# Kernel tuning notes

Measured on AMD Instinct MI355X. Metric: run time of the kernel, lower is better.

The kernel has to match this reference:

```python
import jax, jax.numpy as jnp
import numpy as np

V, I, H = 32000, 512, 1024
B, L, T = 8, 128, 256


def setup_inputs() -> dict:
    key = jax.random.key(0)
    ks = jax.random.split(key, 12)
    s = lambda k, shape, sc: jax.random.normal(k, shape, jnp.float32) * sc
    return {
        "input": jax.random.randint(ks[0], (B, L), 0, V),
        "targets": jax.random.randint(ks[1], (B, T), 0, V),
        "embed_w": s(ks[2], (V, I), 1.0),
        "Wih0": s(ks[3], (3 * H, I), 0.03),
        "Whh0": s(ks[4], (3 * H, H), 0.03),
        "bih0": jnp.zeros((3 * H,), jnp.float32),
        "bhh0": jnp.zeros((3 * H,), jnp.float32),
        "Wih1": s(ks[5], (3 * H, H), 0.03),
        "Whh1": s(ks[6], (3 * H, H), 0.03),
        "bih1": jnp.zeros((3 * H,), jnp.float32),
        "bhh1": jnp.zeros((3 * H,), jnp.float32),
        "Wc": s(ks[7], (H, 2 * H), 0.02),
        "bc": jnp.zeros((H,), jnp.float32),
        "Wv": s(ks[8], (V, H), 0.02),
        "bv": jnp.zeros((V,), jnp.float32),
    }


def _gru_layer(x, Wih, Whh, bih, bhh):
    # x: (B, S, in) -> (B, S, H). PyTorch gate order: r, z, n.
    Bn = x.shape[0]
    Hh = Whh.shape[1]

    def step(h, xt):
        gi = xt @ Wih.T + bih
        gh = h @ Whh.T + bhh
        ir, iz, ig = jnp.split(gi, 3, axis=-1)
        hr, hz, hg = jnp.split(gh, 3, axis=-1)
        r = jax.nn.sigmoid(ir + hr)
        z = jax.nn.sigmoid(iz + hz)
        n = jnp.tanh(ig + r * hg)
        hnew = (1.0 - z) * n + z * h
        return hnew, hnew

    h0 = jnp.zeros((Bn, Hh), x.dtype)
    _, ys = jax.lax.scan(step, h0, jnp.swapaxes(x, 0, 1))
    return jnp.swapaxes(ys, 0, 1)


def reference(input, targets, embed_w, Wih0, Whh0, bih0, bhh0, Wih1, Whh1, bih1, bhh1, Wc, bc, Wv, bv):
    # forcing = 1.0 (fully teacher-forced): GRU inputs = [prompt, targets[:, :-1]]
    Lp = input.shape[1]
    Tt = targets.shape[1]
    toks = jnp.concatenate([input, targets[:, :-1]], axis=1)  # (B, L+T-1)
    emb = embed_w[toks]                                       # (B, L+T-1, I)
    h1 = _gru_layer(emb, Wih0, Whh0, bih0, bhh0)
    O = _gru_layer(h1, Wih1, Whh1, bih1, bhh1)                # (B, L+T-1, H)

    # attention at decode step q: predicted = O[:, L-1+q], previous = O[:, :L-1+q]
    Q = O[:, Lp - 1:, :]                                      # (B, T, H)
    S = jnp.einsum('bqh,bkh->bqk', Q, O)                      # (B, T, L+T-1)
    k_idx = jnp.arange(O.shape[1])
    q_idx = jnp.arange(Tt)
    mask = k_idx[None, :] < (Lp - 1 + q_idx)[:, None]         # strict causal
    S = jnp.where(mask[None], S, -jnp.inf)
    A = jax.nn.softmax(S, axis=-1)
    ctx = jnp.einsum('bqk,bkh->bqh', A, O)                    # (B, T, H)
    comb = jnp.tanh(jnp.concatenate([Q, ctx], axis=-1) @ Wc.T + bc)
    logits = comb @ Wv.T + bv                                 # (B, T, V)
    return logits
```

## Files before the change

### kernel.cpp

```cpp
#include <hip/hip_runtime.h>

typedef __attribute__((ext_vector_type(8))) short bf16x8;
typedef __attribute__((ext_vector_type(4))) float f32x4;

#define GLOAD_LDS16(g, l)                                                     \
  __builtin_amdgcn_global_load_lds(                                           \
      (const __attribute__((address_space(1))) void*)(g),                     \
      (__attribute__((address_space(3))) void*)(l), 16, 0, 0)

#define ALOAD64(p)  __hip_atomic_load((p), __ATOMIC_RELAXED, __HIP_MEMORY_SCOPE_AGENT)
#define ALOADU32(p) __hip_atomic_load((p), __ATOMIC_RELAXED, __HIP_MEMORY_SCOPE_AGENT)
#define ASTOREU32(p, v) __hip_atomic_store((p), (v), __ATOMIC_RELAXED, __HIP_MEMORY_SCOPE_AGENT)

__device__ __forceinline__ unsigned short f2b(float f) {
  union { float f; unsigned int i; } v; v.f = f;
  unsigned int u = v.i;
  u += 0x7fffu + ((u >> 16) & 1u);
  return (unsigned short)(u >> 16);
}
__device__ __forceinline__ float sigm(float x) { return 1.f / (1.f + expf(-x)); }

#define HH   1024
#define H3   3072
#define BB   8
#define SP   384
#define SL   383
#define VV   32000
#define II   512
#define MQ   2048

#define TAG(s) ((unsigned)((s) + 1))

#define CB0 393216
#define CB1 1179648
#define CB2 1966080
#define CB3 2752512
#define CB4 3276800
#define CB5 11468800
__global__ void k_cvt_all(const float* __restrict__ s0, const float* __restrict__ s1,
                          const float* __restrict__ s2, const float* __restrict__ s3,
                          const float* __restrict__ s4, const float* __restrict__ s5,
                          unsigned short* __restrict__ dst) {
  for (int i = blockIdx.x * 256 + threadIdx.x; i < CB5; i += 2048 * 256) {
    const float* src; int o;
    if (i < CB0)      { src = s0; o = i; }
    else if (i < CB1) { src = s1; o = i - CB0; }
    else if (i < CB2) { src = s2; o = i - CB1; }
    else if (i < CB3) { src = s3; o = i - CB2; }
    else if (i < CB4) { src = s4; o = i - CB3; }
    else              { src = s5; o = i - CB4; }
    float4 v = ((const float4*)src)[o];
    ushort4 q;
    q.x = f2b(v.x); q.y = f2b(v.y); q.z = f2b(v.z); q.w = f2b(v.w);
    ((ushort4*)dst)[i] = q;
  }
}

__global__ void k_zero_u32(unsigned int* p, int n) {
  int i = blockIdx.x * 256 + threadIdx.x;
  if (i < n) p[i] = 0u;
}

__global__ void k_embed(const int* __restrict__ input, const int* __restrict__ targets,
                        const float* __restrict__ embed_w, unsigned short* __restrict__ emb) {
  int m = blockIdx.x;
  int b = m / SP, s = m % SP;
  unsigned short* dst = emb + (size_t)m * II;
  if (s == SL) {
    for (int i = threadIdx.x; i < II; i += 256) dst[i] = 0;
    return;
  }
  int tok = (s < 128) ? input[b * 128 + s] : targets[b * 256 + (s - 128)];
  const float* srcw = embed_w + (size_t)tok * II;
  for (int i = threadIdx.x; i < II; i += 256) dst[i] = f2b(srcw[i]);
}

template<bool TANH, bool OUTBF16>
__global__ __launch_bounds__(256) void k_gemm_bt(
    const unsigned short* __restrict__ A, const unsigned short* __restrict__ W,
    const float* __restrict__ bias, void* __restrict__ Cout,
    int M, int N, int K) {
  __shared__ __align__(16) unsigned short As[2][128 * 32];
  __shared__ __align__(16) unsigned short Ws[2][128 * 32];
  const int tid = threadIdx.x;
  const int gx = gridDim.x;
  const int nwg = gx * gridDim.y;
  int orig = blockIdx.y * gx + blockIdx.x;
  int wg = ((nwg & 7) == 0) ? ((orig & 7) * (nwg >> 3) + (orig >> 3)) : orig;
  const int mBase = (wg / gx) * 128, nBase = (wg % gx) * 128;
  const int wid = tid >> 6, lane = tid & 63;
  const int wr = wid >> 1, wc = wid & 1;
  f32x4 acc[4][4];
#pragma unroll
  for (int i = 0; i < 4; ++i)
#pragma unroll
    for (int j = 0; j < 4; ++j) acc[i][j] = (f32x4){0.f, 0.f, 0.f, 0.f};

  const int r0 = tid >> 2, c0 = (tid & 3) * 8;
  const int kq8 = (lane >> 4) * 8;

  auto stage = [&](int kt, int b) {
#pragma unroll
    for (int pass = 0; pass < 2; ++pass) {
      int r = pass * 64 + r0;
      GLOAD_LDS16(A + (size_t)(mBase + r) * K + kt + c0, &As[b][r * 32 + c0]);
      GLOAD_LDS16(W + (size_t)(nBase + r) * K + kt + c0, &Ws[b][r * 32 + c0]);
    }
  };

  stage(0, 0);
  int cur = 0;
  for (int kt = 0; kt < K; kt += 32) {
    asm volatile("s_waitcnt vmcnt(0)" ::: "memory");
    __syncthreads();
    if (kt + 32 < K) stage(kt + 32, cur ^ 1);
    bf16x8 af[4], bfr[4];
#pragma unroll
    for (int mf = 0; mf < 4; ++mf)
      af[mf] = *(const bf16x8*)&As[cur][(wr * 64 + mf * 16 + (lane & 15)) * 32 + kq8];
#pragma unroll
    for (int nf = 0; nf < 4; ++nf)
      bfr[nf] = *(const bf16x8*)&Ws[cur][(wc * 64 + nf * 16 + (lane & 15)) * 32 + kq8];
#pragma unroll
    for (int mf = 0; mf < 4; ++mf)
#pragma unroll
      for (int nf = 0; nf < 4; ++nf)
        acc[mf][nf] = __builtin_amdgcn_mfma_f32_16x16x32_bf16(af[mf], bfr[nf], acc[mf][nf], 0, 0, 0);
    cur ^= 1;
  }
  const int rq = (lane >> 4) * 4;
#pragma unroll
  for (int mf = 0; mf < 4; ++mf) {
#pragma unroll
    for (int nf = 0; nf < 4; ++nf) {
      int n = nBase + wc * 64 + nf * 16 + (lane & 15);
      float bvv = bias[n];
#pragma unroll
      for (int i = 0; i < 4; ++i) {
        int m = mBase + wr * 64 + mf * 16 + rq + i;
        float v = acc[mf][nf][i] + bvv;
        if (TANH) v = tanhf(v);
        if (OUTBF16) ((unsigned short*)Cout)[(size_t)m * N + n] = f2b(v);
        else         ((float*)Cout)[(size_t)m * N + n] = v;
      }
    }
  }
}

__global__ __launch_bounds__(256) void k_obf(const float* __restrict__ O,
                                             unsigned short* __restrict__ Obf,
                                             unsigned short* __restrict__ ObfT) {
  __shared__ unsigned short t[32][33];
  const int b = blockIdx.z, k0 = blockIdx.y * 32, h0 = blockIdx.x * 32;
  const int tx = threadIdx.x & 31, ty = threadIdx.x >> 5;
  const float* Ob = O + ((size_t)b * SP + k0) * 1024 + h0;
#pragma unroll
  for (int i = 0; i < 32; i += 8) {
    unsigned short q = f2b(Ob[(size_t)(ty + i) * 1024 + tx]);
    Obf[((size_t)b * SP + k0 + ty + i) * 1024 + h0 + tx] = q;
    t[ty + i][tx] = q;
  }
  __syncthreads();
#pragma unroll
  for (int i = 0; i < 32; i += 8)
    ObfT[((size_t)b * 1024 + h0 + ty + i) * SP + k0 + tx] = t[tx][ty + i];
}

__global__ void k_qcopy(const unsigned short* __restrict__ Obf,
                        unsigned short* __restrict__ X) {
  int row = blockIdx.x;
  int b = row >> 8, q = row & 255;
  const unsigned* src = (const unsigned*)(Obf + ((size_t)b * SP + 127 + q) * 1024);
  unsigned* dst = (unsigned*)(X + (size_t)row * 2048);
  for (int i = threadIdx.x; i < 512; i += 256) dst[i] = src[i];
}

__global__ __launch_bounds__(256) void k_gemm_qk(
    const unsigned short* __restrict__ Obf, float* __restrict__ Sout) {
  const int b = blockIdx.z;
  const unsigned short* A = Obf + (size_t)b * 393216 + 127 * 1024;
  const unsigned short* W = Obf + (size_t)b * 393216;
  float* Cout = Sout + (size_t)b * 98304;
  const int K = 1024, N = 384;
  __shared__ __align__(16) unsigned short As[2][128 * 32];
  __shared__ __align__(16) unsigned short Ws[2][128 * 32];
  const int tid = threadIdx.x;
  const int mBase = blockIdx.y * 128, nBase = blockIdx.x * 128;
  const int wid = tid >> 6, lane = tid & 63;
  const int wr = wid >> 1, wc = wid & 1;
  f32x4 acc[4][4];
#pragma unroll
  for (int i = 0; i < 4; ++i)
#pragma unroll
    for (int j = 0; j < 4; ++j) acc[i][j] = (f32x4){0.f, 0.f, 0.f, 0.f};
  const int r0 = tid >> 2, c0 = (tid & 3) * 8;
  const int kq8 = (lane >> 4) * 8;
  auto stage = [&](int kt, int bb) {
#pragma unroll
    for (int pass = 0; pass < 2; ++pass) {
      int r = pass * 64 + r0;
      GLOAD_LDS16(A + (size_t)(mBase + r) * K + kt + c0, &As[bb][r * 32 + c0]);
      GLOAD_LDS16(W + (size_t)(nBase + r) * K + kt + c0, &Ws[bb][r * 32 + c0]);
    }
  };
  stage(0, 0);
  int cur = 0;
  for (int kt = 0; kt < K; kt += 32) {
    asm volatile("s_waitcnt vmcnt(0)" ::: "memory");
    __syncthreads();
    if (kt + 32 < K) stage(kt + 32, cur ^ 1);
    bf16x8 af[4], bfr[4];
#pragma unroll
    for (int mf = 0; mf < 4; ++mf)
      af[mf] = *(const bf16x8*)&As[cur][(wr * 64 + mf * 16 + (lane & 15)) * 32 + kq8];
#pragma unroll
    for (int nf = 0; nf < 4; ++nf)
      bfr[nf] = *(const bf16x8*)&Ws[cur][(wc * 64 + nf * 16 + (lane & 15)) * 32 + kq8];
#pragma unroll
    for (int mf = 0; mf < 4; ++mf)
#pragma unroll
      for (int nf = 0; nf < 4; ++nf)
        acc[mf][nf] = __builtin_amdgcn_mfma_f32_16x16x32_bf16(af[mf], bfr[nf], acc[mf][nf], 0, 0, 0);
    cur ^= 1;
  }
  const int rq = (lane >> 4) * 4;
#pragma unroll
  for (int mf = 0; mf < 4; ++mf)
#pragma unroll
    for (int nf = 0; nf < 4; ++nf) {
      int n = nBase + wc * 64 + nf * 16 + (lane & 15);
#pragma unroll
      for (int i = 0; i < 4; ++i) {
        int m = mBase + wr * 64 + mf * 16 + rq + i;
        Cout[(size_t)m * N + n] = acc[mf][nf][i];
      }
    }
}

__global__ __launch_bounds__(64) void k_sm(const float* __restrict__ S,
                                           unsigned short* __restrict__ P) {
  const int row = blockIdx.x;
  const int q = row & 255;
  const int lim = 127 + q;
  const float* Sr = S + (size_t)row * SP;
  unsigned short* Pr = P + (size_t)row * SP;
  const int lane = threadIdx.x;
  float v[6];
  float mx = -INFINITY;
#pragma unroll
  for (int i = 0; i < 6; ++i) {
    int k = lane + i * 64;
    float x = (k < lim) ? Sr[k] : -INFINITY;
    v[i] = x; mx = fmaxf(mx, x);
  }
#pragma unroll
  for (int m = 1; m < 64; m <<= 1) mx = fmaxf(mx, __shfl_xor(mx, m));
  float sum = 0.f;
#pragma unroll
  for (int i = 0; i < 6; ++i) {
    float e = (v[i] == -INFINITY) ? 0.f : expf(v[i] - mx);
    v[i] = e; sum += e;
  }
#pragma unroll
  for (int m = 1; m < 64; m <<= 1) sum += __shfl_xor(sum, m);
  float rinv = 1.f / sum;
#pragma unroll
  for (int i = 0; i < 6; ++i) Pr[lane + i * 64] = f2b(v[i] * rinv);
}

__global__ __launch_bounds__(256) void k_gemm_pv(
    const unsigned short* __restrict__ Pbf, const unsigned short* __restrict__ ObfT,
    unsigned short* __restrict__ X) {
  const int b = blockIdx.z;
  const unsigned short* A = Pbf + (size_t)b * 98304;
  const unsigned short* W = ObfT + (size_t)b * 393216;
  unsigned short* Cout = X + (size_t)(b * 256) * 2048 + 1024;
  const int K = SP, N = 1024;
  __shared__ __align__(16) unsigned short As[2][128 * 32];
  __shared__ __align__(16) unsigned short Ws[2][128 * 32];
  const int tid = threadIdx.x;
  const int mBase = blockIdx.y * 128, nBase = blockIdx.x * 128;
  const int wid = tid >> 6, lane = tid & 63;
  const int wr = wid >> 1, wc = wid & 1;
  f32x4 acc[4][4];
#pragma unroll
  for (int i = 0; i < 4; ++i)
#pragma unroll
    for (int j = 0; j < 4; ++j) acc[i][j] = (f32x4){0.f, 0.f, 0.f, 0.f};
  const int r0 = tid >> 2, c0 = (tid & 3) * 8;
  const int kq8 = (lane >> 4) * 8;
  auto stage = [&](int kt, int bb) {
#pragma unroll
    for (int pass = 0; pass < 2; ++pass) {
      int r = pass * 64 + r0;
      GLOAD_LDS16(A + (size_t)(mBase + r) * K + kt + c0, &As[bb][r * 32 + c0]);
      GLOAD_LDS16(W + (size_t)(nBase + r) * K + kt + c0, &Ws[bb][r * 32 + c0]);
    }
  };
  stage(0, 0);
  int cur = 0;
  for (int kt = 0; kt < K; kt += 32) {
    asm volatile("s_waitcnt vmcnt(0)" ::: "memory");
    __syncthreads();
    if (kt + 32 < K) stage(kt + 32, cur ^ 1);
    bf16x8 af[4], bfr[4];
#pragma unroll
    for (int mf = 0; mf < 4; ++mf)
      af[mf] = *(const bf16x8*)&As[cur][(wr * 64 + mf * 16 + (lane & 15)) * 32 + kq8];
#pragma unroll
    for (int nf = 0; nf < 4; ++nf)
      bfr[nf] = *(const bf16x8*)&Ws[cur][(wc * 64 + nf * 16 + (lane & 15)) * 32 + kq8];
#pragma unroll
    for (int mf = 0; mf < 4; ++mf)
#pragma unroll
      for (int nf = 0; nf < 4; ++nf)
        acc[mf][nf] = __builtin_amdgcn_mfma_f32_16x16x32_bf16(af[mf], bfr[nf], acc[mf][nf], 0, 0, 0);
    cur ^= 1;
  }
  const int rq = (lane >> 4) * 4;
#pragma unroll
  for (int mf = 0; mf < 4; ++mf)
#pragma unroll
    for (int nf = 0; nf < 4; ++nf) {
      int n = nBase + wc * 64 + nf * 16 + (lane & 15);
#pragma unroll
      for (int i = 0; i < 4; ++i) {
        int m = mBase + wr * 64 + mf * 16 + rq + i;
        Cout[(size_t)m * 2048 + n] = f2b(acc[mf][nf][i]);
      }
    }
}

__global__ __launch_bounds__(256) void k_recur(
    const unsigned short* __restrict__ whh0, const unsigned short* __restrict__ wih1,
    const unsigned short* __restrict__ whh1,
    const float* __restrict__ gi0,
    const float* __restrict__ bhh0, const float* __restrict__ bih1,
    const float* __restrict__ bhh1,
    unsigned short* __restrict__ h1g, unsigned short* __restrict__ h2g,
    float* __restrict__ Obuf, unsigned* cnt) {
  extern __shared__ unsigned char smem[];
  unsigned short* wlds  = (unsigned short*)smem;
  unsigned short* hA    = (unsigned short*)(smem + 98304);
  unsigned short* hB    = (unsigned short*)(smem + 114688);
  unsigned short* zrow  = (unsigned short*)(smem + 131072);
  float*          gacc  = (float*)(smem + 133120);

  unsigned* pflag1 = cnt;
  unsigned* pflag2 = cnt + 512;
  unsigned* rflag  = cnt + 1536;

  const int g = blockIdx.x, tid = threadIdx.x;
  const int layer = (g >= 64) ? 1 : 0;
  const int j0 = layer ? (g - 64) * 8 : g * 16;

  for (int p = 0; p < 24; ++p) {
    int c = p * 256 + tid;
    int rr = c >> 7;
    int co = (c & 127) * 8;
    int cs = co ^ ((rr & 7) * 8);
    const unsigned short* src;
    if (layer == 0) {
      int grow = (rr >> 4) * 1024 + j0 + (rr & 15);
      src = whh0 + (size_t)grow * 1024 + cs;
    } else {
      const unsigned short* base; int grow;
      if (rr < 16)      { base = wih1; grow = (rr < 8) ? (j0 + rr) : (1024 + j0 + rr - 8); }
      else if (rr < 32) { base = whh1; int r2 = rr - 16; grow = (r2 < 8) ? (j0 + r2) : (1024 + j0 + r2 - 8); }
      else if (rr < 40) { base = wih1; grow = 2048 + j0 + (rr - 32); }
      else              { base = whh1; grow = 2048 + j0 + (rr - 40); }
      src = base + (size_t)grow * 1024 + cs;
    }
    GLOAD_LDS16(src, wlds + (size_t)rr * 1024 + co);
  }
  {
    ((unsigned int*)zrow)[tid]       = 0u;
    ((unsigned int*)zrow)[tid + 256] = 0u;
    for (int i = tid; i < 1024; i += 256) gacc[i] = 0.f;
  }
  __syncthreads();

  const int w = tid >> 6, lane = tid & 63;
  const int arow = lane & 15, kq8 = (lane >> 4) * 8, bb = lane & 15;

  float c0r = 0.f, c0z = 0.f, c0n = 0.f;
  float c1ir = 0.f, c1iz = 0.f, c1in = 0.f, c1hr = 0.f, c1hz = 0.f, c1hn = 0.f;
  float hprev = 0.f;
  if (layer == 0) {
    if (tid < 128) { int j = j0 + (tid >> 3); c0r = bhh0[j]; c0z = bhh0[1024 + j]; c0n = bhh0[2048 + j]; }
  } else {
    if (tid < 64)  { int j = j0 + (tid >> 3);
      c1ir = bih1[j]; c1iz = bih1[1024 + j]; c1in = bih1[2048 + j];
      c1hr = bhh1[j]; c1hz = bhh1[1024 + j]; c1hn = bhh1[2048 + j]; }
  }

  bool wact; int tb, nrows; int hsel;
  if (layer == 0) { wact = (w < 3); tb = w * 16; nrows = 16; hsel = 0; }
  else { wact = true; tb = (w < 2) ? w * 16 : (32 + (w - 2) * 8); nrows = (w < 2) ? 16 : 8;
         hsel = (w & 1); }
  const unsigned short* abase; int ax;
  if (arow < nrows) { abase = wlds + (size_t)(tb + arow) * 1024; ax = (arow & 7) * 8; }
  else              { abase = zrow; ax = 0; }
  const unsigned short* bbase0; int bx;
  {
    const unsigned short* hX = hsel ? hB : hA;
    if (bb < 8) { bbase0 = hX + (size_t)bb * 1024; bx = (bb & 7) * 8; }
    else        { bbase0 = zrow; bx = 0; }
  }
  const int rq = (lane >> 4) * 4;
  const int kbase = w * 512 + lane;

  for (int s = 0; s < 384; ++s) {
    const bool act = layer ? (s >= 1) : (s <= 382);
    const unsigned short* h1r = h1g + ((s - 1) & 7) * 8192;
    const unsigned short* h2r = h2g + ((s - 2) & 7) * 8192;
    unsigned short* h1w = h1g + (s & 7) * 8192;
    unsigned short* h2w = h2g + ((s - 1) & 7) * 8192;

    float pr = 0.f, pz = 0.f, pn = 0.f;
    if (layer == 0 && act && tid < 128) {
      int cc = tid >> 3, b = tid & 7; int j = j0 + cc;
      size_t m3 = ((size_t)b * SP + s) * H3;
      pr = gi0[m3 + j]; pz = gi0[m3 + 1024 + j]; pn = gi0[m3 + 2048 + j];
    }

    if (w == 0 && act && s >= 1) {
      const unsigned t = TAG(s - 1);
      const bool need2 = (layer == 1) && (s >= 2);
      unsigned* f1 = pflag1 + ((s - 1) & 7) * 64;
      unsigned* f2 = pflag2 + ((s - 1) & 7) * 128;
      for (int it = 0; it < 200000; ++it) {
        int ok = (ALOADU32(f1 + lane) == t);
        if (need2) {
          ok &= (ALOADU32(f2 + lane) == t);
          ok &= (ALOADU32(f2 + 64 + lane) == t);
        }
        if (__all(ok)) break;
        __builtin_amdgcn_s_sleep(1);
      }
    }
    if (w == 1 && (s & 3) == 0 && s >= 4) {
      const unsigned t = TAG(s - 4);
      unsigned* rf = rflag + ((s - 4) & 7) * 192;
      for (int it = 0; it < 100000; ++it) {
        int ok = (ALOADU32(rf + lane) == t)
               & (ALOADU32(rf + 64 + lane) == t)
               & (ALOADU32(rf + 128 + lane) == t);
        if (__all(ok)) break;
        __builtin_amdgcn_s_sleep(1);
      }
    }
    __syncthreads();

    if (act && s >= 1) {
      const unsigned long long* p1 = (const unsigned long long*)h1r;
#pragma unroll
      for (int i = 0; i < 8; ++i) {
        int k = kbase + i * 64;
        unsigned long long v = ALOAD64(p1 + k);
        int b = k >> 8, e = (k & 255) * 4;
        *(unsigned long long*)(hA + b * 1024 + (e ^ (b * 8))) = v;
      }
      if ((layer == 1) && (s >= 2)) {
        const unsigned long long* p2 = (const unsigned long long*)h2r;
#pragma unroll
        for (int i = 0; i < 8; ++i) {
          int k = kbase + i * 64;
          unsigned long long v = ALOAD64(p2 + k);
          int b = k >> 8, e = (k & 255) * 4;
          *(unsigned long long*)(hB + b * 1024 + (e ^ (b * 8))) = v;
        }
      }
    }
    __syncthreads();

    bool domfma = act && wact && (layer == 0 ? (s >= 1) : (hsel == 0 ? (s >= 1) : (s >= 2)));
    if (domfma) {
      f32x4 a0 = (f32x4){0.f, 0.f, 0.f, 0.f};
      f32x4 a1 = (f32x4){0.f, 0.f, 0.f, 0.f};
#pragma unroll
      for (int kt = 0; kt < 32; kt += 2) {
        int ko0 = kt * 32 + kq8, ko1 = ko0 + 32;
        bf16x8 av0 = *(const bf16x8*)(abase + (ko0 ^ ax));
        bf16x8 hv0 = *(const bf16x8*)(bbase0 + (ko0 ^ bx));
        bf16x8 av1 = *(const bf16x8*)(abase + (ko1 ^ ax));
        bf16x8 hv1 = *(const bf16x8*)(bbase0 + (ko1 ^ bx));
        a0 = __builtin_amdgcn_mfma_f32_16x16x32_bf16(av0, hv0, a0, 0, 0, 0);
        a1 = __builtin_amdgcn_mfma_f32_16x16x32_bf16(av1, hv1, a1, 0, 0, 0);
      }
#pragma unroll
      for (int i = 0; i < 4; ++i)
        gacc[w * 256 + (rq + i) * 16 + (lane & 15)] = a0[i] + a1[i];
    }
    __syncthreads();

    if (act) {
      if (layer == 0 && tid < 128) {
        int cc = tid >> 3, b = tid & 7; int j = j0 + cc;
        float gr = pr + gacc[cc * 16 + b]       + c0r;
        float gz = pz + gacc[256 + cc * 16 + b] + c0z;
        float hg =      gacc[512 + cc * 16 + b] + c0n;
        float r = sigm(gr), z = sigm(gz);
        float n = tanhf(pn + r * hg);
        float hn = (1.f - z) * n + z * hprev;
        hprev = hn;
        __hip_atomic_store(h1w + b * 1024 + j, f2b(hn),
                           __ATOMIC_RELAXED, __HIP_MEMORY_SCOPE_AGENT);
      } else if (layer == 1 && tid < 64) {
        int cc = tid >> 3, b = tid & 7; int j = j0 + cc;
        float gr = gacc[cc * 16 + b]       + c1ir + gacc[256 + cc * 16 + b]       + c1hr;
        float gz = gacc[(8 + cc) * 16 + b] + c1iz + gacc[256 + (8 + cc) * 16 + b] + c1hz;
        float gn = gacc[512 + cc * 16 + b] + c1in;
        float hg = gacc[768 + cc * 16 + b] + c1hn;
        float r = sigm(gr), z = sigm(gz);
        float n = tanhf(gn + r * hg);
        float hn = (1.f - z) * n + z * hprev;
        hprev = hn;
        __hip_atomic_store(h2w + b * 1024 + j, f2b(hn),
                           __ATOMIC_RELAXED, __HIP_MEMORY_SCOPE_AGENT);
        Obuf[((size_t)b * SP + (s - 1)) * 1024 + j] = hn;
      }
    }
    asm volatile("s_waitcnt vmcnt(0)" ::: "memory");
    __syncthreads();
    if (act && tid == 0) {
      if (layer == 0) ASTOREU32(pflag1 + (s & 7) * 64 + g, TAG(s));
      else            ASTOREU32(pflag2 + (s & 7) * 128 + (g - 64), TAG(s));
    }
    if (tid == 1) ASTOREU32(rflag + (s & 7) * 192 + g, TAG(s));
  }
}

extern "C" void kernel_launch(void* const* d_in, const int* in_sizes, int n_in,
                              void* d_out, int out_size, void* d_ws, size_t ws_size,
                              hipStream_t stream) {
  (void)in_sizes; (void)n_in; (void)out_size; (void)ws_size;
  const int*   input   = (const int*)d_in[0];
  const int*   targets = (const int*)d_in[1];
  const float* embed_w = (const float*)d_in[2];
  const float* Wih0 = (const float*)d_in[3];
  const float* Whh0 = (const float*)d_in[4];
  const float* bih0 = (const float*)d_in[5];
  const float* bhh0 = (const float*)d_in[6];
  const float* Wih1 = (const float*)d_in[7];
  const float* Whh1 = (const float*)d_in[8];
  const float* bih1 = (const float*)d_in[9];
  const float* bhh1 = (const float*)d_in[10];
  const float* Wc   = (const float*)d_in[11];
  const float* bc   = (const float*)d_in[12];
  const float* Wv   = (const float*)d_in[13];
  const float* bv   = (const float*)d_in[14];
  float* out = (float*)d_out;

  char* ws = (char*)d_ws;
  size_t off = 0;
  auto alloc = [&](size_t bytes) {
    void* p = ws + off; off += (bytes + 255) & ~(size_t)255; return p;
  };
  unsigned short* Wih0b = (unsigned short*)alloc((size_t)H3 * II * 2);
  unsigned short* Whh0b = (unsigned short*)alloc((size_t)H3 * HH * 2);
  unsigned short* Wih1b = (unsigned short*)alloc((size_t)H3 * HH * 2);
  unsigned short* Whh1b = (unsigned short*)alloc((size_t)H3 * HH * 2);
  unsigned short* Wcb   = (unsigned short*)alloc((size_t)HH * 2048 * 2);
  unsigned short* Wvb   = (unsigned short*)alloc((size_t)VV * HH * 2);
  unsigned short* EMBb  = (unsigned short*)alloc((size_t)BB * SP * II * 2);
  float*          GI0   = (float*)alloc((size_t)BB * SP * H3 * 4);
  unsigned short* H1G   = (unsigned short*)alloc(8 * 8192 * 2);
  unsigned short* H2G   = (unsigned short*)alloc(8 * 8192 * 2);
  unsigned*       CNT   = (unsigned*)alloc(3072 * 4);
  float*          OBUF  = (float*)alloc((size_t)BB * SP * HH * 4);
  unsigned short* OBF   = (unsigned short*)alloc((size_t)BB * SP * HH * 2);
  unsigned short* OBFT  = (unsigned short*)alloc((size_t)BB * HH * SP * 2);
  float*          SBUF  = (float*)alloc((size_t)MQ * SP * 4);
  unsigned short* PBF   = (unsigned short*)alloc((size_t)MQ * SP * 2);
  unsigned short* Xb    = (unsigned short*)alloc((size_t)MQ * 2048 * 2);
  unsigned short* COMBb = (unsigned short*)alloc((size_t)MQ * HH * 2);

  k_cvt_all<<<dim3(2048), 256, 0, stream>>>(Wih0, Whh0, Wih1, Whh1, Wc, Wv, Wih0b);

  k_embed<<<dim3(BB * SP), 256, 0, stream>>>(input, targets, embed_w, EMBb);
  k_zero_u32<<<dim3(12), 256, 0, stream>>>((unsigned int*)CNT, 3072);

  k_gemm_bt<false, false><<<dim3(24, 24), 256, 0, stream>>>(
      EMBb, Wih0b, bih0, GI0, BB * SP, H3, II);

  {
    const unsigned short* a0 = Whh0b; const unsigned short* a1 = Wih1b;
    const unsigned short* a2 = Whh1b; const float* a3 = GI0;
    const float* a4 = bhh0; const float* a5 = bih1; const float* a6 = bhh1;
    unsigned short* a7 = H1G; unsigned short* a8 = H2G; float* a9 = OBUF;
    unsigned* a10 = CNT;
    void* args[] = {&a0, &a1, &a2, &a3, &a4, &a5, &a6, &a7, &a8, &a9, &a10};
    hipLaunchCooperativeKernel((void*)k_recur, dim3(192), dim3(256),
                               args, 137216u, stream);
  }

  k_obf<<<dim3(32, 12, 8), 256, 0, stream>>>(OBUF, OBF, OBFT);
  k_qcopy<<<dim3(2048), 256, 0, stream>>>(OBF, Xb);
  k_gemm_qk<<<dim3(3, 2, 8), 256, 0, stream>>>(OBF, SBUF);
  k_sm<<<dim3(2048), 64, 0, stream>>>(SBUF, PBF);
  k_gemm_pv<<<dim3(8, 2, 8), 256, 0, stream>>>(PBF, OBFT, Xb);

  k_gemm_bt<true, true><<<dim3(8, 16), 256, 0, stream>>>(
      Xb, Wcb, bc, COMBb, MQ, HH, 2048);

  k_gemm_bt<false, false><<<dim3(250, 16), 256, 0, stream>>>(
      COMBb, Wvb, bv, out, MQ, VV, HH);
}
```

Before: 2.784 ms.

## Unroll recurrence ring buffers to drop reader flags, fuse qcopy into conversion

The hidden-state and progress-flag ring buffers in the persistent GRU kernel now hold all 384 steps instead of 8 slots. With no slot reuse, the reader-acknowledgement flags (rflag) and their periodic spin-wait are removed from the per-step critical path. The thread-to-(batch, column) mapping in the gate update is changed so adjacent lanes write contiguous columns. The separate k_qcopy kernel is folded into k_obf, which writes the query rows of X directly. The cost is a larger workspace and a bigger flag-zeroing pass.

```diff
diff --git a/kernel.cpp b/kernel.cpp
--- a/kernel.cpp
+++ b/kernel.cpp
@@ -149,30 +149,25 @@
 
 __global__ __launch_bounds__(256) void k_obf(const float* __restrict__ O,
                                              unsigned short* __restrict__ Obf,
-                                             unsigned short* __restrict__ ObfT) {
+                                             unsigned short* __restrict__ ObfT,
+                                             unsigned short* __restrict__ X) {
   __shared__ unsigned short t[32][33];
   const int b = blockIdx.z, k0 = blockIdx.y * 32, h0 = blockIdx.x * 32;
   const int tx = threadIdx.x & 31, ty = threadIdx.x >> 5;
   const float* Ob = O + ((size_t)b * SP + k0) * 1024 + h0;
 #pragma unroll
   for (int i = 0; i < 32; i += 8) {
+    int krow = k0 + ty + i;
     unsigned short q = f2b(Ob[(size_t)(ty + i) * 1024 + tx]);
-    Obf[((size_t)b * SP + k0 + ty + i) * 1024 + h0 + tx] = q;
+    Obf[((size_t)b * SP + krow) * 1024 + h0 + tx] = q;
+    if (krow >= 127 && krow < 383)
+      X[((size_t)(b * 256 + krow - 127)) * 2048 + h0 + tx] = q;
     t[ty + i][tx] = q;
   }
   __syncthreads();
 #pragma unroll
   for (int i = 0; i < 32; i += 8)
     ObfT[((size_t)b * 1024 + h0 + ty + i) * SP + k0 + tx] = t[tx][ty + i];
-}
-
-__global__ void k_qcopy(const unsigned short* __restrict__ Obf,
-                        unsigned short* __restrict__ X) {
-  int row = blockIdx.x;
-  int b = row >> 8, q = row & 255;
-  const unsigned* src = (const unsigned*)(Obf + ((size_t)b * SP + 127 + q) * 1024);
-  unsigned* dst = (unsigned*)(X + (size_t)row * 2048);
-  for (int i = threadIdx.x; i < 512; i += 256) dst[i] = src[i];
 }
 
 __global__ __launch_bounds__(256) void k_gemm_qk(
@@ -347,8 +342,7 @@
   float*          gacc  = (float*)(smem + 133120);
 
   unsigned* pflag1 = cnt;
-  unsigned* pflag2 = cnt + 512;
-  unsigned* rflag  = cnt + 1536;
+  unsigned* pflag2 = cnt + 384 * 64;
 
   const int g = blockIdx.x, tid = threadIdx.x;
   const int layer = (g >= 64) ? 1 : 0;
@@ -387,9 +381,10 @@
   float c1ir = 0.f, c1iz = 0.f, c1in = 0.f, c1hr = 0.f, c1hz = 0.f, c1hn = 0.f;
   float hprev = 0.f;
   if (layer == 0) {
-    if (tid < 128) { int j = j0 + (tid >> 3); c0r = bhh0[j]; c0z = bhh0[1024 + j]; c0n = bhh0[2048 + j]; }
+    if (tid < 128) { int j = j0 + (tid & 15);
+      c0r = bhh0[j]; c0z = bhh0[1024 + j]; c0n = bhh0[2048 + j]; }
   } else {
-    if (tid < 64)  { int j = j0 + (tid >> 3);
+    if (tid < 64)  { int j = j0 + (tid & 7);
       c1ir = bih1[j]; c1iz = bih1[1024 + j]; c1in = bih1[2048 + j];
       c1hr = bhh1[j]; c1hz = bhh1[1024 + j]; c1hn = bhh1[2048 + j]; }
   }
@@ -412,14 +407,14 @@
 
   for (int s = 0; s < 384; ++s) {
     const bool act = layer ? (s >= 1) : (s <= 382);
-    const unsigned short* h1r = h1g + ((s - 1) & 7) * 8192;
-    const unsigned short* h2r = h2g + ((s - 2) & 7) * 8192;
-    unsigned short* h1w = h1g + (s & 7) * 8192;
-    unsigned short* h2w = h2g + ((s - 1) & 7) * 8192;
+    const unsigned short* h1r = h1g + (size_t)(s - 1) * 8192;
+    const unsigned short* h2r = h2g + (size_t)(s - 2) * 8192;
+    unsigned short* h1w = h1g + (size_t)s * 8192;
+    unsigned short* h2w = h2g + (size_t)(s - 1) * 8192;
 
     float pr = 0.f, pz = 0.f, pn = 0.f;
     if (layer == 0 && act && tid < 128) {
-      int cc = tid >> 3, b = tid & 7; int j = j0 + cc;
+      int b = tid >> 4, j = j0 + (tid & 15);
       size_t m3 = ((size_t)b * SP + s) * H3;
       pr = gi0[m3 + j]; pz = gi0[m3 + 1024 + j]; pn = gi0[m3 + 2048 + j];
     }
@@ -427,8 +422,8 @@
     if (w == 0 && act && s >= 1) {
       const unsigned t = TAG(s - 1);
       const bool need2 = (layer == 1) && (s >= 2);
-      unsigned* f1 = pflag1 + ((s - 1) & 7) * 64;
-      unsigned* f2 = pflag2 + ((s - 1) & 7) * 128;
+      unsigned* f1 = pflag1 + (s - 1) * 64;
+      unsigned* f2 = pflag2 + (s - 1) * 128;
       for (int it = 0; it < 200000; ++it) {
         int ok = (ALOADU32(f1 + lane) == t);
         if (need2) {
@@ -439,17 +434,6 @@
         __builtin_amdgcn_s_sleep(1);
       }
     }
-    if (w == 1 && (s & 3) == 0 && s >= 4) {
-      const unsigned t = TAG(s - 4);
-      unsigned* rf = rflag + ((s - 4) & 7) * 192;
-      for (int it = 0; it < 100000; ++it) {
-        int ok = (ALOADU32(rf + lane) == t)
-               & (ALOADU32(rf + 64 + lane) == t)
-               & (ALOADU32(rf + 128 + lane) == t);
-        if (__all(ok)) break;
-        __builtin_amdgcn_s_sleep(1);
-      }
-    }
     __syncthreads();
 
     if (act && s >= 1) {
@@ -496,7 +480,7 @@
 
     if (act) {
       if (layer == 0 && tid < 128) {
-        int cc = tid >> 3, b = tid & 7; int j = j0 + cc;
+        int b = tid >> 4, cc = tid & 15; int j = j0 + cc;
         float gr = pr + gacc[cc * 16 + b]       + c0r;
         float gz = pz + gacc[256 + cc * 16 + b] + c0z;
         float hg =      gacc[512 + cc * 16 + b] + c0n;
@@ -507,7 +491,7 @@
         __hip_atomic_store(h1w + b * 1024 + j, f2b(hn),
                            __ATOMIC_RELAXED, __HIP_MEMORY_SCOPE_AGENT);
       } else if (layer == 1 && tid < 64) {
-        int cc = tid >> 3, b = tid & 7; int j = j0 + cc;
+        int b = tid >> 3, cc = tid & 7; int j = j0 + cc;
         float gr = gacc[cc * 16 + b]       + c1ir + gacc[256 + cc * 16 + b]       + c1hr;
         float gz = gacc[(8 + cc) * 16 + b] + c1iz + gacc[256 + (8 + cc) * 16 + b] + c1hz;
         float gn = gacc[512 + cc * 16 + b] + c1in;
@@ -524,10 +508,9 @@
     asm volatile("s_waitcnt vmcnt(0)" ::: "memory");
     __syncthreads();
     if (act && tid == 0) {
-      if (layer == 0) ASTOREU32(pflag1 + (s & 7) * 64 + g, TAG(s));
-      else            ASTOREU32(pflag2 + (s & 7) * 128 + (g - 64), TAG(s));
-    }
-    if (tid == 1) ASTOREU32(rflag + (s & 7) * 192 + g, TAG(s));
+      if (layer == 0) ASTOREU32(pflag1 + s * 64 + g, TAG(s));
+      else            ASTOREU32(pflag2 + s * 128 + (g - 64), TAG(s));
+    }
   }
 }
 
@@ -565,9 +548,9 @@
   unsigned short* Wvb   = (unsigned short*)alloc((size_t)VV * HH * 2);
   unsigned short* EMBb  = (unsigned short*)alloc((size_t)BB * SP * II * 2);
   float*          GI0   = (float*)alloc((size_t)BB * SP * H3 * 4);
-  unsigned short* H1G   = (unsigned short*)alloc(8 * 8192 * 2);
-  unsigned short* H2G   = (unsigned short*)alloc(8 * 8192 * 2);
-  unsigned*       CNT   = (unsigned*)alloc(3072 * 4);
+  unsigned short* H1G   = (unsigned short*)alloc((size_t)384 * 8192 * 2);
+  unsigned short* H2G   = (unsigned short*)alloc((size_t)384 * 8192 * 2);
+  unsigned*       CNT   = (unsigned*)alloc((size_t)(384 * 64 + 384 * 128) * 4);
   float*          OBUF  = (float*)alloc((size_t)BB * SP * HH * 4);
   unsigned short* OBF   = (unsigned short*)alloc((size_t)BB * SP * HH * 2);
   unsigned short* OBFT  = (unsigned short*)alloc((size_t)BB * HH * SP * 2);
@@ -579,7 +562,7 @@
   k_cvt_all<<<dim3(2048), 256, 0, stream>>>(Wih0, Whh0, Wih1, Whh1, Wc, Wv, Wih0b);
 
   k_embed<<<dim3(BB * SP), 256, 0, stream>>>(input, targets, embed_w, EMBb);
-  k_zero_u32<<<dim3(12), 256, 0, stream>>>((unsigned int*)CNT, 3072);
+  k_zero_u32<<<dim3(288), 256, 0, stream>>>((unsigned int*)CNT, 73728);
 
   k_gemm_bt<false, false><<<dim3(24, 24), 256, 0, stream>>>(
       EMBb, Wih0b, bih0, GI0, BB * SP, H3, II);
@@ -595,8 +578,7 @@
                                args, 137216u, stream);
   }
 
-  k_obf<<<dim3(32, 12, 8), 256, 0, stream>>>(OBUF, OBF, OBFT);
-  k_qcopy<<<dim3(2048), 256, 0, stream>>>(OBF, Xb);
+  k_obf<<<dim3(32, 12, 8), 256, 0, stream>>>(OBUF, OBF, OBFT, Xb);
   k_gemm_qk<<<dim3(3, 2, 8), 256, 0, stream>>>(OBF, SBUF);
   k_sm<<<dim3(2048), 64, 0, stream>>>(SBUF, PBF);
   k_gemm_pv<<<dim3(8, 2, 8), 256, 0, stream>>>(PBF, OBFT, Xb);
```

Result: slower. 2.935 ms (+5.4%).
